# Kernel optimization log

Measured on AMD Instinct MI355X. Metric: run time of the kernel, lower is better.

## Reference

```python
import jax, jax.numpy as jnp
import numpy as np

B, L, D, H, K = 4, 2048, 1024, 16, 256
DH = D // H
SCALE = DH ** -0.5


def setup_inputs() -> dict:
    key = jax.random.key(0)
    ks = jax.random.split(key, 8)
    std = 1.0 / np.sqrt(D)
    pstd = 1.0 / np.sqrt(K)  # init_ uses last dim of (seq_len, k) tensor
    return {
        "x": jax.random.normal(ks[0], (B, L, D), dtype=jnp.float32),
        "Wq": jax.random.uniform(ks[1], (D, D), jnp.float32, -std, std),
        "Wk": jax.random.uniform(ks[2], (D, D), jnp.float32, -std, std),
        "Wv": jax.random.uniform(ks[3], (D, D), jnp.float32, -std, std),
        "proj_k": jax.random.uniform(ks[4], (L, K), jnp.float32, -pstd, pstd),
        "proj_v": jax.random.uniform(ks[5], (L, K), jnp.float32, -pstd, pstd),
        "Wo": jax.random.uniform(ks[6], (D, D), jnp.float32, -std, std),
        "bo": jax.random.uniform(ks[7], (D,), jnp.float32, -std, std),
    }


def reference(x, Wq, Wk, Wv, proj_k, proj_v, Wo, bo):
    b, l, d = x.shape
    q = x @ Wq.T                                   # [B,L,D]
    keys = jnp.einsum("bnd,nk->bkd", x @ Wk.T, proj_k)   # [B,K,D]
    vals = jnp.einsum("bnd,nk->bkd", x @ Wv.T, proj_v)   # [B,K,D]
    # faithful to original: plain reshape (B,h,L,d_h), NOT transpose-split
    q = q.reshape(b, H, l, DH)
    k = keys.reshape(b, K, H, DH).transpose(0, 2, 1, 3)  # [B,H,K,DH]
    v = vals.reshape(b, K, H, DH).transpose(0, 2, 1, 3)  # [B,H,K,DH]
    attn = jax.nn.softmax(jnp.einsum("bhld,bhkd->bhlk", q, k) * SCALE, axis=-1)
    out = jnp.einsum("bhlk,bhkd->bhld", attn, v)
    out = out.transpose(0, 2, 1, 3).reshape(b, l, d)
    return out @ Wo.T + bo
```

## Files before the change

### kernel.cpp

```cpp
#include <hip/hip_runtime.h>


typedef __attribute__((ext_vector_type(8))) short short8;
typedef __attribute__((ext_vector_type(4))) short short4_t;
typedef __attribute__((ext_vector_type(4))) float facc;

#define B_    4
#define L_    2048
#define D_    1024
#define H_    16
#define KP    256
#define DH_   64
#define SCALE_ 0.125f

__device__ __forceinline__ short f2b(float f) {
  unsigned u = __float_as_uint(f);
  unsigned r = (u + 0x7fffu + ((u >> 16) & 1u)) >> 16;
  return (short)r;
}

__device__ __forceinline__ void load16_to_lds(const short* gp, short* lp) {
  __builtin_amdgcn_global_load_lds(
      (const __attribute__((address_space(1))) void*)gp,
      (__attribute__((address_space(3))) void*)lp, 16, 0, 0);
}

__global__ void castW(const float* __restrict__ w0, const float* __restrict__ w1,
                      const float* __restrict__ w2, const float* __restrict__ w3,
                      short* __restrict__ dst) {
  const int z = blockIdx.y;
  const float* s = (z == 0) ? w0 : (z == 1) ? w1 : (z == 2) ? w2 : w3;
  int i = (blockIdx.x * blockDim.x + threadIdx.x) * 4;
  float4 f = *(const float4*)(s + i);
  short4_t v; v[0] = f2b(f.x); v[1] = f2b(f.y); v[2] = f2b(f.z); v[3] = f2b(f.w);
  *(short4_t*)(dst + (size_t)z * 1048576 + i) = v;
}

__global__ void transX(const float* __restrict__ x, short* __restrict__ xb,
                       short* __restrict__ xTb) {
  __shared__ float tl[32][33];
  const int b = blockIdx.z;
  const float* s = x + (size_t)b * L_ * D_;
  int c0 = blockIdx.x * 32, r0 = blockIdx.y * 32;
  int tx = threadIdx.x, ty = threadIdx.y;
#pragma unroll
  for (int i = 0; i < 32; i += 8) {
    float v = s[(size_t)(r0 + ty + i) * D_ + c0 + tx];
    tl[ty + i][tx] = v;
    xb[(size_t)b * L_ * D_ + (size_t)(r0 + ty + i) * D_ + c0 + tx] = f2b(v);
  }
  __syncthreads();
#pragma unroll
  for (int i = 0; i < 32; i += 8)
    xTb[(size_t)b * D_ * L_ + (size_t)(c0 + ty + i) * L_ + r0 + tx] = f2b(tl[tx][ty + i]);
}

__global__ void projTm(const float* __restrict__ pk, const float* __restrict__ pv,
                       short* __restrict__ dst) {
  __shared__ float tl[32][33];
  const int z = blockIdx.z;
  const float* s = z ? pv : pk;
  short* d = dst + (size_t)z * (KP * L_);
  int c0 = blockIdx.x * 32, r0 = blockIdx.y * 32;
  int tx = threadIdx.x, ty = threadIdx.y;
#pragma unroll
  for (int i = 0; i < 32; i += 8)
    tl[ty + i][tx] = s[(size_t)(r0 + ty + i) * KP + c0 + tx];
  __syncthreads();
#pragma unroll
  for (int i = 0; i < 32; i += 8)
    d[(size_t)(c0 + ty + i) * L_ + r0 + tx] = f2b(tl[tx][ty + i]);
}

__global__ void transVals(const short* __restrict__ src, short* __restrict__ dst) {
  __shared__ short tl[32][33];
  int z = blockIdx.z; int b = z >> 4, h = z & 15;
  const short* s = src + (size_t)b * KP * D_ + h * DH_;
  short* d = dst + (size_t)z * DH_ * KP;
  int d0 = blockIdx.x * 32, kp0 = blockIdx.y * 32;
  int tx = threadIdx.x, ty = threadIdx.y;
#pragma unroll
  for (int i = 0; i < 32; i += 8)
    tl[ty + i][tx] = s[(size_t)(kp0 + ty + i) * D_ + d0 + tx];
  __syncthreads();
#pragma unroll
  for (int i = 0; i < 32; i += 8)
    d[(size_t)(d0 + ty + i) * KP + kp0 + tx] = tl[tx][ty + i];
}

template<int TM, int TN, int NC, bool SWZ>
__global__ __launch_bounds__(256) void gemm_lds(
    const short* __restrict__ Am, const short* __restrict__ Bm,
    const float* __restrict__ bias, float* __restrict__ C32,
    short* __restrict__ Cb, int M, int N, int K,
    long aHi, long aLo, long bHi, long bLo, long cHi, long cLo, int zDiv)
{
  constexpr int MT = TM / 32, NT = TN / 32;
  __shared__ __attribute__((aligned(16))) short As[NC][TM * 32];
  __shared__ __attribute__((aligned(16))) short Bs[NC][TN * 32];
  const int t = threadIdx.x, lane = t & 63, w = t >> 6;
  const int lm = lane & 15, g = lane >> 4;
  const int z = blockIdx.z, zhi = z / zDiv, zlo = z % zDiv;
  int bm, bn;
  if (SWZ) {
    const int p = blockIdx.y * 8 + blockIdx.x;
    bn = (p >> 3) & 7;
    bm = ((p >> 6) << 3) | (p & 7);
  } else {
    bm = blockIdx.y; bn = blockIdx.x;
  }
  const int m0 = bm * TM, n0 = bn * TN;
  const int wm = (w & 1) * (TM / 2), wn = (w >> 1) * (TN / 2);

  const short* Ab = Am + zhi * aHi + zlo * aLo;
  const short* Bp = Bm + zhi * bHi + zlo * bLo;

  facc acc[MT][NT];
  const facc fz = {0.f, 0.f, 0.f, 0.f};
#pragma unroll
  for (int i = 0; i < MT; i++)
#pragma unroll
    for (int j = 0; j < NT; j++) acc[i][j] = fz;

  const int lrow = lane >> 2;
  const int lch  = (lane & 3) * 8;

  for (int k0 = 0; k0 < K; k0 += 32 * NC) {
    __syncthreads();
#pragma unroll
    for (int c = 0; c < NC; c++) {
#pragma unroll
      for (int rnd = 0; rnd < TM / 64; rnd++) {
        const int row = rnd * 64 + w * 16;
        load16_to_lds(Ab + (size_t)(m0 + row + lrow) * K + k0 + c * 32 + lch,
                      &As[c][row * 32]);
      }
#pragma unroll
      for (int rnd = 0; rnd < TN / 64; rnd++) {
        const int row = rnd * 64 + w * 16;
        load16_to_lds(Bp + (size_t)(n0 + row + lrow) * K + k0 + c * 32 + lch,
                      &Bs[c][row * 32]);
      }
    }
    __syncthreads();

#pragma unroll
    for (int c = 0; c < NC; c++) {
      short8 af[MT], bf[NT];
#pragma unroll
      for (int mt = 0; mt < MT; mt++)
        af[mt] = *(const short8*)(&As[c][(wm + 16 * mt + lm) * 32 + g * 8]);
#pragma unroll
      for (int nt = 0; nt < NT; nt++)
        bf[nt] = *(const short8*)(&Bs[c][(wn + 16 * nt + lm) * 32 + g * 8]);
#pragma unroll
      for (int mt = 0; mt < MT; mt++)
#pragma unroll
        for (int nt = 0; nt < NT; nt++)
          acc[mt][nt] = __builtin_amdgcn_mfma_f32_16x16x32_bf16(af[mt], bf[nt], acc[mt][nt], 0, 0, 0);
    }
  }

  const long cz = zhi * cHi + zlo * cLo;
#pragma unroll
  for (int mt = 0; mt < MT; mt++)
#pragma unroll
    for (int r = 0; r < 4; r++) {
      const int row = m0 + wm + 16 * mt + 4 * g + r;
#pragma unroll
      for (int nt = 0; nt < NT; nt++) {
        const int col = n0 + wn + 16 * nt + lm;
        float v = acc[mt][nt][r];
        if (bias) v += bias[col];
        if (C32) C32[cz + (size_t)row * N + col] = v;
        if (Cb)  Cb[cz + (size_t)row * N + col] = f2b(v);
      }
    }
}

__global__ __launch_bounds__(256) void attn_mfma(
    const short* __restrict__ xqb, const short* __restrict__ keysb,
    const short* __restrict__ vTb, short* __restrict__ out2b)
{
  __shared__ __attribute__((aligned(16))) short Kt[2][64 * 72];
  __shared__ __attribute__((aligned(16))) short Vt[2][64 * 72];
  __shared__ __attribute__((aligned(16))) short Pt[4][32 * 72];

  const int t = threadIdx.x, lane = t & 63, w = t >> 6;
  const int lm = lane & 15, g = lane >> 4;
  const int b = blockIdx.z, h = blockIdx.y;
  const int l0w = blockIdx.x * 128 + w * 32;

  short8 aq[2][2];
#pragma unroll
  for (int mt = 0; mt < 2; mt++) {
    const int l = l0w + 16 * mt + lm;
    const short* qrow = xqb + ((size_t)b * L_ + h * 128 + (l >> 4)) * D_ + (l & 15) * DH_;
#pragma unroll
    for (int ks = 0; ks < 2; ks++)
      aq[mt][ks] = *(const short8*)(qrow + ks * 32 + g * 8);
  }

  facc accO[2][4];
  const facc fz = {0.f, 0.f, 0.f, 0.f};
#pragma unroll
  for (int mt = 0; mt < 2; mt++)
#pragma unroll
    for (int dt = 0; dt < 4; dt++) accO[mt][dt] = fz;
  float lrow[2][4];
#pragma unroll
  for (int mt = 0; mt < 2; mt++)
#pragma unroll
    for (int r = 0; r < 4; r++) lrow[mt][r] = 0.f;

  const short* Kb = keysb + (size_t)b * KP * D_ + h * DH_;
  const short* Vb = vTb + ((size_t)b * H_ + h) * DH_ * KP;

  const int srow = t >> 3, sch = (t & 7) * 8;

#pragma unroll
  for (int i = 0; i < 2; i++) {
    const int row = srow + 32 * i;
    *(short8*)(&Kt[0][row * 72 + sch]) = *(const short8*)(Kb + (size_t)row * D_ + sch);
    *(short8*)(&Vt[0][row * 72 + sch]) = *(const short8*)(Vb + (size_t)row * KP + sch);
  }
  __syncthreads();

  for (int c = 0; c < 4; c++) {
    const int bi = c & 1;
    if (c < 3) {
#pragma unroll
      for (int i = 0; i < 2; i++) {
        const int row = srow + 32 * i;
        *(short8*)(&Kt[bi ^ 1][row * 72 + sch]) =
            *(const short8*)(Kb + (size_t)((c + 1) * 64 + row) * D_ + sch);
        *(short8*)(&Vt[bi ^ 1][row * 72 + sch]) =
            *(const short8*)(Vb + (size_t)row * KP + (c + 1) * 64 + sch);
      }
    }

    facc S[2][4];
#pragma unroll
    for (int mt = 0; mt < 2; mt++)
#pragma unroll
      for (int nt = 0; nt < 4; nt++) S[mt][nt] = fz;
#pragma unroll
    for (int ks = 0; ks < 2; ks++) {
      short8 bk[4];
#pragma unroll
      for (int nt = 0; nt < 4; nt++)
        bk[nt] = *(const short8*)(&Kt[bi][(16 * nt + lm) * 72 + ks * 32 + g * 8]);
#pragma unroll
      for (int mt = 0; mt < 2; mt++)
#pragma unroll
        for (int nt = 0; nt < 4; nt++)
          S[mt][nt] = __builtin_amdgcn_mfma_f32_16x16x32_bf16(aq[mt][ks], bk[nt], S[mt][nt], 0, 0, 0);
    }

#pragma unroll
    for (int mt = 0; mt < 2; mt++)
#pragma unroll
      for (int r = 0; r < 4; r++) {
        float ps = 0.f;
        const int prow = (16 * mt + 4 * g + r) * 72;
#pragma unroll
        for (int nt = 0; nt < 4; nt++) {
          const float p = __expf(S[mt][nt][r] * SCALE_);
          ps += p;
          Pt[w][prow + 16 * nt + lm] = f2b(p);
        }
        lrow[mt][r] += ps;
      }

#pragma unroll
    for (int ks = 0; ks < 2; ks++) {
      short8 ap[2], bv[4];
#pragma unroll
      for (int mt = 0; mt < 2; mt++)
        ap[mt] = *(const short8*)(&Pt[w][(16 * mt + lm) * 72 + ks * 32 + g * 8]);
#pragma unroll
      for (int dt = 0; dt < 4; dt++)
        bv[dt] = *(const short8*)(&Vt[bi][(16 * dt + lm) * 72 + ks * 32 + g * 8]);
#pragma unroll
      for (int mt = 0; mt < 2; mt++)
#pragma unroll
        for (int dt = 0; dt < 4; dt++)
          accO[mt][dt] = __builtin_amdgcn_mfma_f32_16x16x32_bf16(ap[mt], bv[dt], accO[mt][dt], 0, 0, 0);
    }
    __syncthreads();
  }

#pragma unroll
  for (int mt = 0; mt < 2; mt++)
#pragma unroll
    for (int r = 0; r < 4; r++) {
      float ls = lrow[mt][r];
      ls += __shfl_xor(ls, 1);
      ls += __shfl_xor(ls, 2);
      ls += __shfl_xor(ls, 4);
      ls += __shfl_xor(ls, 8);
      const float inv = 1.0f / ls;
      const int l = l0w + 16 * mt + 4 * g + r;
#pragma unroll
      for (int dt = 0; dt < 4; dt++)
        out2b[((size_t)b * L_ + l) * D_ + h * DH_ + 16 * dt + lm] = f2b(accO[mt][dt][r] * inv);
    }
}

extern "C" void kernel_launch(void* const* d_in, const int* in_sizes, int n_in,
                              void* d_out, int out_size, void* d_ws, size_t ws_size,
                              hipStream_t stream)
{
  const float* x      = (const float*)d_in[0];
  const float* Wq     = (const float*)d_in[1];
  const float* Wk     = (const float*)d_in[2];
  const float* Wv     = (const float*)d_in[3];
  const float* proj_k = (const float*)d_in[4];
  const float* proj_v = (const float*)d_in[5];
  const float* Wo     = (const float*)d_in[6];
  const float* bo     = (const float*)d_in[7];
  float* out = (float*)d_out;

  short* ws     = (short*)d_ws;
  short* xqb    = ws;
  short* xTb    = xqb    + 8388608;
  short* xb     = xTb    + 8388608;
  short* out2b  = xb;
  short* Wqb    = xb     + 8388608;
  short* Wkb    = Wqb    + 1048576;
  short* Wvb    = Wkb    + 1048576;
  short* Wob    = Wvb    + 1048576;
  short* projTk = Wob    + 1048576;
  short* projTv = projTk + 524288;
  short* xk2b   = projTv + 524288;
  short* xv2b   = xk2b   + 1048576;
  short* keysb  = xv2b   + 1048576;
  short* valsb  = keysb  + 1048576;
  short* vT     = valsb  + 1048576;
  (void)Wkb; (void)Wvb; (void)projTv; (void)xv2b;

  castW<<<dim3(1024, 4), 256, 0, stream>>>(Wq, Wk, Wv, Wo, Wqb);
  transX<<<dim3(32, 64, 4), dim3(32, 8), 0, stream>>>(x, xb, xTb);
  projTm<<<dim3(8, 64, 2), dim3(32, 8), 0, stream>>>(proj_k, proj_v, projTk);

  gemm_lds<128, 128, 2, true><<<dim3(8, 64, 1), 256, 0, stream>>>(
      xb, Wqb, nullptr, nullptr, xqb, 8192, 1024, 1024, 0, 0, 0, 0, 0, 0, 1);

  gemm_lds<64, 64, 2, false><<<dim3(16, 4, 8), 256, 0, stream>>>(
      projTk, xTb, nullptr, nullptr, xk2b, 256, 1024, 2048,
      524288, 0, 0, (long)D_ * L_, 1048576, 262144, 4);

  gemm_lds<64, 64, 2, false><<<dim3(16, 16, 2), 256, 0, stream>>>(
      xk2b, Wkb, nullptr, nullptr, keysb, 1024, 1024, 1024,
      1048576, 0, 1048576, 0, 1048576, 0, 1);

  transVals<<<dim3(2, 8, 64), dim3(32, 8), 0, stream>>>(valsb, vT);

  attn_mfma<<<dim3(16, 16, 4), 256, 0, stream>>>(xqb, keysb, vT, out2b);

  gemm_lds<128, 128, 2, true><<<dim3(8, 64, 1), 256, 0, stream>>>(
      out2b, Wob, bo, out, nullptr, 8192, 1024, 1024, 0, 0, 0, 0, 0, 0, 1);
}
```

Baseline: 239.8 us.

## Merge prep kernels into one launch and fuse value transpose into GEMM epilogue

Folds the weight cast, x transpose/cast and projection transpose into a single prepX kernel that reads float4 per thread. The value GEMM now writes its output straight into the transposed per-head vT layout from its epilogue, so the separate transVals kernel and the valsb buffer write go away. This cuts three kernel launches and one round trip through global memory. The cost is a large grid with many early-exit blocks and scattered 8-byte transposed stores in the GEMM epilogue.

```diff
diff --git a/kernel.cpp b/kernel.cpp
--- a/kernel.cpp
+++ b/kernel.cpp
@@ -25,74 +25,62 @@
       (__attribute__((address_space(3))) void*)lp, 16, 0, 0);
 }
 
-__global__ void castW(const float* __restrict__ w0, const float* __restrict__ w1,
-                      const float* __restrict__ w2, const float* __restrict__ w3,
-                      short* __restrict__ dst) {
-  const int z = blockIdx.y;
-  const float* s = (z == 0) ? w0 : (z == 1) ? w1 : (z == 2) ? w2 : w3;
-  int i = (blockIdx.x * blockDim.x + threadIdx.x) * 4;
-  float4 f = *(const float4*)(s + i);
-  short4_t v; v[0] = f2b(f.x); v[1] = f2b(f.y); v[2] = f2b(f.z); v[3] = f2b(f.w);
-  *(short4_t*)(dst + (size_t)z * 1048576 + i) = v;
-}
-
-__global__ void transX(const float* __restrict__ x, short* __restrict__ xb,
-                       short* __restrict__ xTb) {
-  __shared__ float tl[32][33];
-  const int b = blockIdx.z;
-  const float* s = x + (size_t)b * L_ * D_;
-  int c0 = blockIdx.x * 32, r0 = blockIdx.y * 32;
-  int tx = threadIdx.x, ty = threadIdx.y;
-#pragma unroll
-  for (int i = 0; i < 32; i += 8) {
-    float v = s[(size_t)(r0 + ty + i) * D_ + c0 + tx];
-    tl[ty + i][tx] = v;
-    xb[(size_t)b * L_ * D_ + (size_t)(r0 + ty + i) * D_ + c0 + tx] = f2b(v);
-  }
-  __syncthreads();
-#pragma unroll
-  for (int i = 0; i < 32; i += 8)
-    xTb[(size_t)b * D_ * L_ + (size_t)(c0 + ty + i) * L_ + r0 + tx] = f2b(tl[tx][ty + i]);
-}
-
-__global__ void projTm(const float* __restrict__ pk, const float* __restrict__ pv,
-                       short* __restrict__ dst) {
-  __shared__ float tl[32][33];
-  const int z = blockIdx.z;
-  const float* s = z ? pv : pk;
-  short* d = dst + (size_t)z * (KP * L_);
-  int c0 = blockIdx.x * 32, r0 = blockIdx.y * 32;
-  int tx = threadIdx.x, ty = threadIdx.y;
-#pragma unroll
-  for (int i = 0; i < 32; i += 8)
-    tl[ty + i][tx] = s[(size_t)(r0 + ty + i) * KP + c0 + tx];
-  __syncthreads();
-#pragma unroll
-  for (int i = 0; i < 32; i += 8)
-    d[(size_t)(c0 + ty + i) * L_ + r0 + tx] = f2b(tl[tx][ty + i]);
-}
-
-__global__ void transVals(const short* __restrict__ src, short* __restrict__ dst) {
-  __shared__ short tl[32][33];
-  int z = blockIdx.z; int b = z >> 4, h = z & 15;
-  const short* s = src + (size_t)b * KP * D_ + h * DH_;
-  short* d = dst + (size_t)z * DH_ * KP;
-  int d0 = blockIdx.x * 32, kp0 = blockIdx.y * 32;
-  int tx = threadIdx.x, ty = threadIdx.y;
-#pragma unroll
-  for (int i = 0; i < 32; i += 8)
-    tl[ty + i][tx] = s[(size_t)(kp0 + ty + i) * D_ + d0 + tx];
-  __syncthreads();
-#pragma unroll
-  for (int i = 0; i < 32; i += 8)
-    d[(size_t)(d0 + ty + i) * KP + kp0 + tx] = tl[tx][ty + i];
+__global__ __launch_bounds__(256) void prepX(
+    const float* __restrict__ x,  const float* __restrict__ pk,
+    const float* __restrict__ pv, const float* __restrict__ w0,
+    const float* __restrict__ w1, const float* __restrict__ w2,
+    const float* __restrict__ w3, short* __restrict__ xb,
+    short* __restrict__ xTb, short* __restrict__ projT,
+    short* __restrict__ Wb)
+{
+  const int z = blockIdx.z, tid = threadIdx.x;
+  if (z >= 6) {
+    const int bid  = blockIdx.y * 32 + blockIdx.x;
+    const int widx = (z - 6) * 2 + (bid >> 10);
+    const float* s = (widx == 0) ? w0 : (widx == 1) ? w1 : (widx == 2) ? w2 : w3;
+    const int i = ((bid & 1023) * 256 + tid) * 4;
+    float4 f = *(const float4*)(s + i);
+    short4_t v; v[0] = f2b(f.x); v[1] = f2b(f.y); v[2] = f2b(f.z); v[3] = f2b(f.w);
+    *(short4_t*)(Wb + (size_t)widx * 1048576 + i) = v;
+    return;
+  }
+
+  __shared__ float tl[32][37];
+  const int row = tid >> 3, c4 = tid & 7;
+
+  if (z < 4) {
+    const int b = z, l0 = blockIdx.y * 32, d0 = blockIdx.x * 32;
+    const float* s = x + (size_t)b * L_ * D_;
+    float4 f = *(const float4*)(s + (size_t)(l0 + row) * D_ + d0 + c4 * 4);
+    short4_t v; v[0] = f2b(f.x); v[1] = f2b(f.y); v[2] = f2b(f.z); v[3] = f2b(f.w);
+    *(short4_t*)(xb + (size_t)b * L_ * D_ + (size_t)(l0 + row) * D_ + d0 + c4 * 4) = v;
+    tl[row][c4 * 4 + 0] = f.x; tl[row][c4 * 4 + 1] = f.y;
+    tl[row][c4 * 4 + 2] = f.z; tl[row][c4 * 4 + 3] = f.w;
+    __syncthreads();
+    short4_t t;
+#pragma unroll
+    for (int j = 0; j < 4; j++) t[j] = f2b(tl[c4 * 4 + j][row]);
+    *(short4_t*)(xTb + (size_t)b * D_ * L_ + (size_t)(d0 + row) * L_ + l0 + c4 * 4) = t;
+  } else {
+    if (blockIdx.x >= 8) return;
+    const int sel = z - 4, l0 = blockIdx.y * 32, k0 = blockIdx.x * 32;
+    const float* s = sel ? pv : pk;
+    float4 f = *(const float4*)(s + (size_t)(l0 + row) * KP + k0 + c4 * 4);
+    tl[row][c4 * 4 + 0] = f.x; tl[row][c4 * 4 + 1] = f.y;
+    tl[row][c4 * 4 + 2] = f.z; tl[row][c4 * 4 + 3] = f.w;
+    __syncthreads();
+    short4_t t;
+#pragma unroll
+    for (int j = 0; j < 4; j++) t[j] = f2b(tl[c4 * 4 + j][row]);
+    *(short4_t*)(projT + (size_t)sel * (KP * L_) + (size_t)(k0 + row) * L_ + l0 + c4 * 4) = t;
+  }
 }
 
 template<int TM, int TN, int NC, bool SWZ>
 __global__ __launch_bounds__(256) void gemm_lds(
     const short* __restrict__ Am, const short* __restrict__ Bm,
     const float* __restrict__ bias, float* __restrict__ C32,
-    short* __restrict__ Cb, int M, int N, int K,
+    short* __restrict__ Cb, short* __restrict__ CbT, int M, int N, int K,
     long aHi, long aLo, long bHi, long bLo, long cHi, long cLo, int zDiv)
 {
   constexpr int MT = TM / 32, NT = TN / 32;
@@ -159,6 +147,24 @@
         for (int nt = 0; nt < NT; nt++)
           acc[mt][nt] = __builtin_amdgcn_mfma_f32_16x16x32_bf16(af[mt], bf[nt], acc[mt][nt], 0, 0, 0);
     }
+  }
+
+  if (CbT && zhi == 1) {
+#pragma unroll
+    for (int mt = 0; mt < MT; mt++) {
+      const int rb = m0 + wm + 16 * mt + 4 * g;
+      const size_t bb = (size_t)(rb >> 8) * (16 * 64 * 256);
+      const int kp = rb & 255;
+#pragma unroll
+      for (int nt = 0; nt < NT; nt++) {
+        const int col = n0 + wn + 16 * nt + lm;
+        short4_t o4;
+#pragma unroll
+        for (int r = 0; r < 4; r++) o4[r] = f2b(acc[mt][nt][r]);
+        *(short4_t*)(CbT + bb + (size_t)col * KP + kp) = o4;
+      }
+    }
+    return;
   }
 
   const long cz = zhi * cHi + zlo * cLo;
@@ -337,27 +343,26 @@
   short* keysb  = xv2b   + 1048576;
   short* valsb  = keysb  + 1048576;
   short* vT     = valsb  + 1048576;
-  (void)Wkb; (void)Wvb; (void)projTv; (void)xv2b;
-
-  castW<<<dim3(1024, 4), 256, 0, stream>>>(Wq, Wk, Wv, Wo, Wqb);
-  transX<<<dim3(32, 64, 4), dim3(32, 8), 0, stream>>>(x, xb, xTb);
-  projTm<<<dim3(8, 64, 2), dim3(32, 8), 0, stream>>>(proj_k, proj_v, projTk);
+  (void)Wkb; (void)Wvb; (void)projTv; (void)xv2b; (void)valsb;
+
+  prepX<<<dim3(32, 64, 8), 256, 0, stream>>>(
+      x, proj_k, proj_v, Wq, Wk, Wv, Wo, xb, xTb, projTk, Wqb);
 
   gemm_lds<128, 128, 2, true><<<dim3(8, 64, 1), 256, 0, stream>>>(
-      xb, Wqb, nullptr, nullptr, xqb, 8192, 1024, 1024, 0, 0, 0, 0, 0, 0, 1);
+      xb, Wqb, nullptr, nullptr, xqb, nullptr, 8192, 1024, 1024,
+      0, 0, 0, 0, 0, 0, 1);
 
   gemm_lds<64, 64, 2, false><<<dim3(16, 4, 8), 256, 0, stream>>>(
-      projTk, xTb, nullptr, nullptr, xk2b, 256, 1024, 2048,
+      projTk, xTb, nullptr, nullptr, xk2b, nullptr, 256, 1024, 2048,
       524288, 0, 0, (long)D_ * L_, 1048576, 262144, 4);
 
   gemm_lds<64, 64, 2, false><<<dim3(16, 16, 2), 256, 0, stream>>>(
-      xk2b, Wkb, nullptr, nullptr, keysb, 1024, 1024, 1024,
-      1048576, 0, 1048576, 0, 1048576, 0, 1);
-
-  transVals<<<dim3(2, 8, 64), dim3(32, 8), 0, stream>>>(valsb, vT);
+      xk2b, Wkb, nullptr, nullptr, keysb, vT, 1024, 1024, 1024,
+      1048576, 0, 1048576, 0, 0, 0, 1);
 
   attn_mfma<<<dim3(16, 16, 4), 256, 0, stream>>>(xqb, keysb, vT, out2b);
 
   gemm_lds<128, 128, 2, true><<<dim3(8, 64, 1), 256, 0, stream>>>(
-      out2b, Wob, bo, out, nullptr, 8192, 1024, 1024, 0, 0, 0, 0, 0, 0, 1);
-}
+      out2b, Wob, bo, out, nullptr, nullptr, 8192, 1024, 1024,
+      0, 0, 0, 0, 0, 0, 1);
+}
```

After: 232.5 us. 3.0% less time.
